# Kernel tuning notes

Measured on AMD Instinct MI355X. Metric: run time of the kernel, lower is better.

The kernel has to match this reference:

```python
import jax, jax.numpy as jnp
import numpy as np

N, T = 128, 20
E_IN, E_EMB, E_RNN = 2, 64, 256
N_IN, N_EMB, N_RNN, N_OUT = 2, 64, 128, 5
ATT = 64

# static edge index sets: diagonal = temporal edges (i,i), off-diagonal = spatial edges (i,j)
_DIAG = np.arange(N) * N + np.arange(N)
_OFFJ = np.array([[j for j in range(N) if j != i] for i in range(N)])  # [N, N-1]
_OFFD = (np.arange(N)[:, None] * N + _OFFJ).reshape(-1)               # [N*(N-1)]
_TEMP = (N - 1) / np.sqrt(ATT)  # attention temperature = num_edges / sqrt(attention_size)


def setup_inputs() -> dict:
    ks = iter(jax.random.split(jax.random.key(0), 40))
    def p(shape, s=0.05):
        return jax.random.normal(next(ks), shape, jnp.float32) * s
    return {
        "nodes": p((T, N, N_IN), 1.0),
        "edges": p((T, N * N, E_IN), 1.0),
        "h_edge0": jnp.zeros((N * N, E_RNN), jnp.float32),
        "c_edge0": jnp.zeros((N * N, E_RNN), jnp.float32),
        "h_node0": jnp.zeros((N, N_RNN), jnp.float32),
        "c_node0": jnp.zeros((N, N_RNN), jnp.float32),
        "t_enc_w": p((E_EMB, E_IN)), "t_enc_b": p((E_EMB,)),
        "t_wih": p((4 * E_RNN, E_EMB)), "t_whh": p((4 * E_RNN, E_RNN)),
        "t_bih": p((4 * E_RNN,)), "t_bhh": p((4 * E_RNN,)),
        "s_enc_w": p((E_EMB, E_IN)), "s_enc_b": p((E_EMB,)),
        "s_wih": p((4 * E_RNN, E_EMB)), "s_whh": p((4 * E_RNN, E_RNN)),
        "s_bih": p((4 * E_RNN,)), "s_bhh": p((4 * E_RNN,)),
        "att_t_w": p((ATT, E_RNN)), "att_t_b": p((ATT,)),
        "att_s_w": p((ATT, E_RNN)), "att_s_b": p((ATT,)),
        "n_enc_w": p((N_EMB, N_IN)), "n_enc_b": p((N_EMB,)),
        "n_attn_w": p((N_EMB, 2 * E_RNN)), "n_attn_b": p((N_EMB,)),
        "n_wih": p((4 * N_RNN, 2 * N_EMB)), "n_whh": p((4 * N_RNN, N_RNN)),
        "n_bih": p((4 * N_RNN,)), "n_bhh": p((4 * N_RNN,)),
        "out_w": p((N_OUT, N_RNN)), "out_b": p((N_OUT,)),
    }


def _lstm(x, h, c, wih, whh, bih, bhh):
    g = x @ wih.T + bih + h @ whh.T + bhh
    i, f, gg, o = jnp.split(g, 4, axis=-1)
    c2 = jax.nn.sigmoid(f) * c + jax.nn.sigmoid(i) * jnp.tanh(gg)
    return jax.nn.sigmoid(o) * jnp.tanh(c2), c2


def reference(nodes, edges, h_edge0, c_edge0, h_node0, c_node0,
              t_enc_w, t_enc_b, t_wih, t_whh, t_bih, t_bhh,
              s_enc_w, s_enc_b, s_wih, s_whh, s_bih, s_bhh,
              att_t_w, att_t_b, att_s_w, att_s_b,
              n_enc_w, n_enc_b, n_attn_w, n_attn_b,
              n_wih, n_whh, n_bih, n_bhh, out_w, out_b):
    def step(carry, xt):
        h_e, c_e, h_n, c_n = carry
        pos_t, edg_t = xt
        # temporal edge RNN on self edges (i,i)
        x_t = jax.nn.relu(edg_t[_DIAG] @ t_enc_w.T + t_enc_b)
        h_t, c_t = _lstm(x_t, h_e[_DIAG], c_e[_DIAG], t_wih, t_whh, t_bih, t_bhh)
        # spatial edge RNN on all pairwise edges (i,j), i != j
        x_s = jax.nn.relu(edg_t[_OFFD] @ s_enc_w.T + s_enc_b)
        h_s, c_s = _lstm(x_s, h_e[_OFFD], c_e[_OFFD], s_wih, s_whh, s_bih, s_bhh)
        h_e = h_e.at[_DIAG].set(h_t).at[_OFFD].set(h_s)
        c_e = c_e.at[_DIAG].set(c_t).at[_OFFD].set(c_s)
        # attention: each node attends over its N-1 spatial edge hidden states
        hs = h_s.reshape(N, N - 1, E_RNN)
        te = h_t @ att_t_w.T + att_t_b                          # [N, ATT]
        se = jnp.einsum('nkd,ad->nka', hs, att_s_w) + att_s_b   # [N, N-1, ATT]
        logits = jnp.einsum('nka,na->nk', se, te) * _TEMP
        w = jax.nn.softmax(logits, axis=-1)
        weighted = jnp.einsum('nk,nkd->nd', w, hs)              # [N, E_RNN]
        # node RNN
        enc = jax.nn.relu(pos_t @ n_enc_w.T + n_enc_b)
        h_edges = jnp.concatenate([h_t, weighted], axis=-1)
        h_emb = jax.nn.relu(h_edges @ n_attn_w.T + n_attn_b)
        h_n, c_n = _lstm(jnp.concatenate([enc, h_emb], axis=-1), h_n, c_n,
                         n_wih, n_whh, n_bih, n_bhh)
        out = h_n @ out_w.T + out_b
        return (h_e, c_e, h_n, c_n), out

    _, outs = jax.lax.scan(step, (h_edge0, c_edge0, h_node0, c_node0), (nodes, edges))
    return outs  # [T, N, 5]
```

## Files before the change

kernel.cpp:

```cpp
#include <hip/hip_runtime.h>
#include <cmath>

#define NN 128
#define TT 20
#define ERNN 256
#define TEMPSC 15.875f

typedef __attribute__((ext_vector_type(8))) short bf16x8;
typedef __attribute__((ext_vector_type(4))) float f32x4;

__device__ __forceinline__ float sigm(float x){ return 1.f/(1.f+__expf(-x)); }
__device__ __forceinline__ float b2f(unsigned short u){ union{unsigned int i; float f;} v; v.i = ((unsigned int)u)<<16; return v.f; }
__device__ __forceinline__ unsigned short f2b(float x){ union{float f; unsigned int u;} v; v.f = x; unsigned int r = v.u + 0x7fffu + ((v.u>>16)&1u); return (unsigned short)(r>>16); }

typedef __attribute__((address_space(3))) unsigned int lds_u32;
typedef __attribute__((address_space(1))) unsigned int glb_u32;
__device__ __forceinline__ void glds16(const void* g, void* l){
    __builtin_amdgcn_global_load_lds((const glb_u32*)g, (lds_u32*)l, 16, 0, 0);
}

__device__ __forceinline__ size_t hoff(int r, int d){
    return ((size_t)((r>>7)*32 + (d>>3))*128 + (r&127))*8 + (d&7);
}

__global__ void k_transpose(const float* __restrict__ s, float* __restrict__ d, int R, int C){
    int i = blockIdx.x*256 + threadIdx.x;
    if (i < R*C){ int r = i / C, c = i - r*C; d[c*R + r] = s[i]; }
}

__global__ void k_bias_sum(const float* __restrict__ a, const float* __restrict__ b,
                           float* __restrict__ o, int n){
    int i = blockIdx.x*256 + threadIdx.x;
    if (i < n) o[i] = a[i] + b[i];
}

__global__ void k_prep_w(const float* __restrict__ wih, const float* __restrict__ whh,
                         unsigned short* __restrict__ wHi){
    int idx = blockIdx.x*256 + threadIdx.x;
    if (idx >= 1024*320) return;
    int c = idx / 320, k = idx - c*320;
    int ch = ((c>>6)<<4) + (c&15), g = (c>>4)&3;
    int r = g*256 + ch;
    float v = (k < 64) ? wih[r*64 + k] : whh[r*256 + (k-64)];
    size_t dst = ((size_t)((c>>7)*40 + (k>>3))*128 + (c&127))*8 + (k&7);
    wHi[dst] = f2b(v);
}

__global__ void k_prep_b(const float* __restrict__ bih, const float* __restrict__ bhh,
                         float* __restrict__ bs){
    int c = blockIdx.x*256 + threadIdx.x;
    if (c < 1024){ int ch = ((c>>6)<<4)+(c&15), g=(c>>4)&3; int r = g*256+ch; bs[c] = bih[r] + bhh[r]; }
}

__global__ void k_prep_xenc(const float* __restrict__ edges,
                            const float* __restrict__ s_enc_w, const float* __restrict__ s_enc_b,
                            const float* __restrict__ t_enc_w, const float* __restrict__ t_enc_b,
                            unsigned short* __restrict__ xe){
    size_t g = (size_t)blockIdx.x*256 + threadIdx.x;
    if (g >= (size_t)TT*16384*8) return;
    int row = (int)(g & 127);
    size_t rest = g >> 7;
    int kc = (int)(rest & 7);
    int tile = (int)((rest >> 3) & 127);
    int t = (int)(rest >> 10);
    int r = tile*128 + row;
    bool sp = (r < 16256);
    int row_ij;
    if (sp) { int i = r/127, jj = r - i*127; row_ij = i*NN + jj + (jj>=i ? 1:0); }
    else    { row_ij = (r - 16256)*(NN+1); }
    const float* w = sp ? s_enc_w : t_enc_w;
    const float* b = sp ? s_enc_b : t_enc_b;
    float e0 = edges[((size_t)t*16384 + row_ij)*2];
    float e1 = edges[((size_t)t*16384 + row_ij)*2 + 1];
    bf16x8 v8;
    #pragma unroll
    for (int q = 0; q < 8; ++q) {
        int m = kc*8 + q;
        v8[q] = (short)f2b(fmaxf(fmaf(w[m*2], e0, fmaf(w[m*2+1], e1, b[m])), 0.f));
    }
    *(bf16x8*)&xe[g*8] = v8;
}

__global__ void k_init_state(const float* __restrict__ h0, const float* __restrict__ c0,
                             unsigned short* __restrict__ hHi, float* __restrict__ c_all){
    int g = blockIdx.x*256 + threadIdx.x;
    if (g >= 16384*32) return;
    int d8 = g & 31, r = g >> 5;
    int row_ij;
    if (r < 16256){ int i = r/127, jj = r - i*127; row_ij = i*NN + jj + (jj>=i ? 1:0); }
    else          { row_ij = (r - 16256)*(NN+1); }
    const float* hs = h0 + (size_t)row_ij*ERNN + d8*8;
    const float* cs = c0 + (size_t)row_ij*ERNN + d8*8;
    bf16x8 hb;
    #pragma unroll
    for (int q = 0; q < 8; ++q) hb[q] = (short)f2b(hs[q]);
    *(bf16x8*)&hHi[hoff(r, d8*8)] = hb;
    float* cd = c_all + (size_t)r*ERNN + d8*8;
    *(float4*)cd       = *(const float4*)cs;
    *(float4*)(cd + 4) = *(const float4*)(cs + 4);
}

__global__ __launch_bounds__(512) void k_fused(
    const unsigned short* __restrict__ xenc_t,
    const unsigned short* __restrict__ h_in, unsigned short* __restrict__ h_out,
    unsigned short* __restrict__ hl_out, float* __restrict__ c_all,
    const unsigned short* __restrict__ s_wHi, const float* __restrict__ s_bs,
    const unsigned short* __restrict__ t_wHi, const float* __restrict__ t_bs,
    int has_node, int n_edge,
    const float* __restrict__ nodes_prev, const unsigned short* __restrict__ hl_prev,
    float* __restrict__ h_nn, float* __restrict__ c_nn, float* __restrict__ out_prev,
    const float* __restrict__ att_t_w, const float* __restrict__ att_t_b,
    const float* __restrict__ att_s_w, const float* __restrict__ att_s_b,
    const float* __restrict__ n_enc_w, const float* __restrict__ n_enc_b,
    const float* __restrict__ n_attn_w, const float* __restrict__ n_attn_b,
    const float* __restrict__ n_wT, const float* __restrict__ n_bsum,
    const float* __restrict__ out_w, const float* __restrict__ out_b)
{
    __shared__ __align__(16) char smem[16384];
    const int bid = blockIdx.x, tid = threadIdx.x;

    if (bid < NN) {
        if (!has_node) return;
        const int i = bid;
        float* sm  = (float*)smem;
        float* ht  = sm;
        float* te  = sm + 256;
        float* u   = sm + 320;
        float* lg  = sm + 576;
        float* cat = sm + 704;
        float* xc  = sm + 1216;
        float* hnl = sm + 1344;
        float* gl  = sm + 1472;
        float* pws = sm + 1984;
        float* msc = sm + 4032;

        if (tid < 256) ht[tid] = b2f(hl_prev[(size_t)(16256 + i)*256 + tid]);
        __syncthreads();
        if (tid < 256) {
            int m = tid >> 2, q = tid & 3;
            float s = 0.f;
            const float* wr = att_t_w + m*ERNN + q*64;
            const float* hh = ht + q*64;
            #pragma unroll 8
            for (int k = 0; k < 64; ++k) s = fmaf(wr[k], hh[k], s);
            s += __shfl_xor(s, 1);
            s += __shfl_xor(s, 2);
            if (q == 0) te[m] = s + att_t_b[m];
        }
        __syncthreads();
        if (tid < 256) {
            float s = 0.f;
            for (int m = 0; m < 64; ++m) s = fmaf(att_s_w[m*ERNN + tid], te[m], s);
            u[tid] = s;
        }
        if (tid == 320) {
            float s = 0.f;
            for (int m = 0; m < 64; ++m) s = fmaf(te[m], att_s_b[m], s);
            msc[2] = s;
        }
        __syncthreads();
        {
            int slot = tid >> 2, q = tid & 3;
            float part = 0.f;
            if (slot < 127) {
                const unsigned short* hs = hl_prev + (size_t)(i*127 + slot)*256 + q*64;
                const float* uu = u + q*64;
                #pragma unroll
                for (int d8 = 0; d8 < 8; ++d8) {
                    bf16x8 v = *(const bf16x8*)(hs + d8*8);
                    #pragma unroll
                    for (int j = 0; j < 8; ++j)
                        part = fmaf(uu[d8*8 + j], b2f((unsigned short)v[j]), part);
                }
            }
            part += __shfl_xor(part, 1);
            part += __shfl_xor(part, 2);
            if (slot < 127 && q == 0) lg[slot] = (part + msc[2]) * TEMPSC;
            if (tid == 511) lg[127] = -1e30f;
        }
        __syncthreads();
        if (tid < 64) {
            float a = fmaxf(lg[tid], lg[tid+64]);
            for (int off = 32; off; off >>= 1) a = fmaxf(a, __shfl_xor(a, off));
            if (tid == 0) msc[0] = a;
        }
        __syncthreads();
        if (tid < 128) lg[tid] = (tid < 127) ? __expf(lg[tid] - msc[0]) : 0.f;
        __syncthreads();
        if (tid < 64) {
            float a = lg[tid] + lg[tid+64];
            for (int off = 32; off; off >>= 1) a += __shfl_xor(a, off);
            if (tid == 0) msc[1] = a;
        }
        __syncthreads();
        {
            int w = tid >> 6, lane = tid & 63;
            float a0 = 0.f, a1 = 0.f, a2 = 0.f, a3 = 0.f;
            #pragma unroll 4
            for (int s = w*16; s < w*16 + 16; ++s) {
                int srow = (s < 127) ? s : 0;
                float wgt = lg[s];
                const unsigned short* hs = hl_prev + (size_t)(i*127 + srow)*256 + lane*4;
                ushort4 v = *(const ushort4*)hs;
                a0 = fmaf(wgt, b2f(v.x), a0);
                a1 = fmaf(wgt, b2f(v.y), a1);
                a2 = fmaf(wgt, b2f(v.z), a2);
                a3 = fmaf(wgt, b2f(v.w), a3);
            }
            pws[w*256 + lane*4+0] = a0; pws[w*256 + lane*4+1] = a1;
            pws[w*256 + lane*4+2] = a2; pws[w*256 + lane*4+3] = a3;
        }
        if (tid >= 256 && tid < 384) hnl[tid-256] = h_nn[i*128 + (tid-256)];
        __syncthreads();
        if (tid < 256) {
            float s = 0.f;
            #pragma unroll
            for (int w = 0; w < 8; ++w) s += pws[w*256 + tid];
            cat[256 + tid] = s / msc[1];
            cat[tid] = ht[tid];
        }
        __syncthreads();
        if (tid < 64) {
            float p0 = nodes_prev[i*2], p1 = nodes_prev[i*2+1];
            xc[tid] = fmaxf(fmaf(n_enc_w[tid*2], p0, fmaf(n_enc_w[tid*2+1], p1, n_enc_b[tid])), 0.f);
        }
        if (tid >= 256) {
            int t2 = tid - 256;
            int m = t2 >> 2, q = t2 & 3;
            float s = 0.f;
            const float* wr = n_attn_w + m*512 + q*128;
            const float* cc = cat + q*128;
            #pragma unroll 8
            for (int d = 0; d < 128; ++d) s = fmaf(wr[d], cc[d], s);
            s += __shfl_xor(s, 1);
            s += __shfl_xor(s, 2);
            if (q == 0) xc[64 + m] = fmaxf(s + n_attn_b[m], 0.f);
        }
        __syncthreads();
        {
            int n = tid;
            float s = n_bsum[n];
            for (int k = 0; k < 128; ++k) s = fmaf(n_wT[k*512 + n], xc[k], s);
            for (int k = 0; k < 128; ++k) s = fmaf(n_wT[(128+k)*512 + n], hnl[k], s);
            gl[n] = s;
        }
        __syncthreads();
        if (tid < 128) {
            float co = c_nn[i*128 + tid];
            float c2 = sigm(gl[128+tid])*co + sigm(gl[tid])*tanhf(gl[256+tid]);
            float h2 = sigm(gl[384+tid])*tanhf(c2);
            c_nn[i*128+tid] = c2;
            h_nn[i*128+tid] = h2;
            hnl[tid] = h2;
        }
        __syncthreads();
        if (tid < 5) {
            float s = out_b[tid];
            const float* wr = out_w + tid*128;
            for (int k = 0; k < 128; ++k) s = fmaf(wr[k], hnl[k], s);
            out_prev[i*5 + tid] = s;
        }
        return;
    }

    if (!n_edge) return;
    unsigned short* Ah = (unsigned short*)smem;
    unsigned short* Bh = (unsigned short*)(smem + 8192);
    const int ebid = bid - NN;
    const int lane = tid & 63, wid = tid >> 6;
    const int wg = (ebid & 7)*128 + (ebid >> 3);
    const int bm = wg >> 3, ntp = wg & 7;
    const bool sp = (bm < 127);
    const int rbase = bm * 128;
    const unsigned short* wHi = sp ? s_wHi : t_wHi;
    const float* bs = sp ? s_bs : t_bs;
    const int wr = wid & 3, wc = wid >> 2;
    const int nt = ntp*2 + wc;

    auto stage = [&](int ks){
        int kc = wid >> 1, half = wid & 1;
        const unsigned short* asrc = (ks < 2)
            ? xenc_t + ((size_t)bm*8  + ks*4     + kc)*1024 + half*512
            : h_in   + ((size_t)bm*32 + (ks-2)*4 + kc)*1024 + half*512;
        glds16(asrc + lane*8, (char*)Ah + wid*1024);
        size_t wb = ((size_t)(ntp*40 + ks*4 + kc)*128 + half*64)*8;
        glds16(wHi + wb + lane*8, (char*)Bh + wid*1024);
    };
    stage(0);

    f32x4 acc[2][4];
    #pragma unroll
    for (int m = 0; m < 2; ++m)
        #pragma unroll
        for (int g = 0; g < 4; ++g)
            acc[m][g] = (f32x4){0.f,0.f,0.f,0.f};

    const int arow = wr*32 + (lane & 15);
    const int bcol = wc*64 + (lane & 15);
    const int kg = lane >> 4;
    for (int ks = 0; ; ++ks) {
        __syncthreads();
        bf16x8 a[2], bb[4];
        #pragma unroll
        for (int m = 0; m < 2; ++m) a[m] = *(const bf16x8*)&Ah[(kg*128 + arow + m*16)*8];
        #pragma unroll
        for (int g = 0; g < 4; ++g) bb[g] = *(const bf16x8*)&Bh[(kg*128 + bcol + g*16)*8];
        #pragma unroll
        for (int m = 0; m < 2; ++m)
            #pragma unroll
            for (int g = 0; g < 4; ++g)
                acc[m][g] = __builtin_amdgcn_mfma_f32_16x16x32_bf16(a[m], bb[g], acc[m][g], 0, 0, 0);
        if (ks == 9) break;
        __syncthreads();
        stage(ks+1);
    }

    const int chl = lane & 15, q4 = (lane >> 4)*4;
    const int ch = nt*16 + chl;
    const int cbase = nt*64 + chl;
    const float b0 = bs[cbase], b1 = bs[cbase+16], b2 = bs[cbase+32], b3 = bs[cbase+48];
    #pragma unroll
    for (int m = 0; m < 2; ++m) {
        #pragma unroll
        for (int rg = 0; rg < 4; ++rg) {
            int lrow = wr*32 + m*16 + q4 + rg;
            int row = rbase + lrow;
            float gi = acc[m][0][rg] + b0;
            float gf = acc[m][1][rg] + b1;
            float gg = acc[m][2][rg] + b2;
            float go = acc[m][3][rg] + b3;
            size_t off = (size_t)row*256 + ch;
            float c_old = c_all[off];
            float c2 = sigm(gf)*c_old + sigm(gi)*tanhf(gg);
            float h2 = sigm(go)*tanhf(c2);
            c_all[off] = c2;
            unsigned short hb = f2b(h2);
            h_out[((size_t)(bm*32 + (ch>>3))*128 + lrow)*8 + (ch&7)] = hb;
            hl_out[off] = hb;
        }
    }
}

extern "C" void kernel_launch(void* const* d_in, const int* in_sizes, int n_in,
                              void* d_out, int out_size, void* d_ws, size_t ws_size,
                              hipStream_t stream)
{
    const float* nodes   = (const float*)d_in[0];
    const float* edges   = (const float*)d_in[1];
    const float* h_e0    = (const float*)d_in[2];
    const float* c_e0    = (const float*)d_in[3];
    const float* h_n0    = (const float*)d_in[4];
    const float* c_n0    = (const float*)d_in[5];
    const float* t_enc_w = (const float*)d_in[6];
    const float* t_enc_b = (const float*)d_in[7];
    const float* t_wih   = (const float*)d_in[8];
    const float* t_whh   = (const float*)d_in[9];
    const float* t_bih   = (const float*)d_in[10];
    const float* t_bhh   = (const float*)d_in[11];
    const float* s_enc_w = (const float*)d_in[12];
    const float* s_enc_b = (const float*)d_in[13];
    const float* s_wih   = (const float*)d_in[14];
    const float* s_whh   = (const float*)d_in[15];
    const float* s_bih   = (const float*)d_in[16];
    const float* s_bhh   = (const float*)d_in[17];
    const float* att_t_w = (const float*)d_in[18];
    const float* att_t_b = (const float*)d_in[19];
    const float* att_s_w = (const float*)d_in[20];
    const float* att_s_b = (const float*)d_in[21];
    const float* n_enc_w = (const float*)d_in[22];
    const float* n_enc_b = (const float*)d_in[23];
    const float* n_attn_w= (const float*)d_in[24];
    const float* n_attn_b= (const float*)d_in[25];
    const float* n_wih   = (const float*)d_in[26];
    const float* n_whh   = (const float*)d_in[27];
    const float* n_bih   = (const float*)d_in[28];
    const float* n_bhh   = (const float*)d_in[29];
    const float* out_w   = (const float*)d_in[30];
    const float* out_b   = (const float*)d_in[31];
    float* out = (float*)d_out;

    char* p = (char*)d_ws;
    float* c_all = (float*)p;            p += (size_t)16384*256*4;
    float* h_nn  = (float*)p;            p += 128*128*4;
    float* c_nn  = (float*)p;            p += 128*128*4;
    float* s_bs  = (float*)p;            p += 1024*4;
    float* t_bs  = (float*)p;            p += 1024*4;
    float* n_wT  = (float*)p;            p += 256*512*4;
    float* n_bs  = (float*)p;            p += 512*4;
    unsigned short* h_a  = (unsigned short*)p;  p += (size_t)16384*256*2;
    unsigned short* h_b  = (unsigned short*)p;  p += (size_t)16384*256*2;
    unsigned short* hl_a = (unsigned short*)p;  p += (size_t)16384*256*2;
    unsigned short* hl_b = (unsigned short*)p;  p += (size_t)16384*256*2;
    unsigned short* xenc = (unsigned short*)p;  p += (size_t)TT*16384*64*2;
    unsigned short* s_wHi = (unsigned short*)p; p += 1024*320*2;
    unsigned short* t_wHi = (unsigned short*)p; p += 1024*320*2;

    hipMemcpyAsync(h_nn, h_n0, 128*128*sizeof(float), hipMemcpyDeviceToDevice, stream);
    hipMemcpyAsync(c_nn, c_n0, 128*128*sizeof(float), hipMemcpyDeviceToDevice, stream);

    k_init_state<<<2048, 256, 0, stream>>>(h_e0, c_e0, h_a, c_all);
    k_prep_w<<<1280, 256, 0, stream>>>(s_wih, s_whh, s_wHi);
    k_prep_w<<<1280, 256, 0, stream>>>(t_wih, t_whh, t_wHi);
    k_prep_b<<<4, 256, 0, stream>>>(s_bih, s_bhh, s_bs);
    k_prep_b<<<4, 256, 0, stream>>>(t_bih, t_bhh, t_bs);
    k_prep_xenc<<<10240, 256, 0, stream>>>(edges, s_enc_w, s_enc_b, t_enc_w, t_enc_b, xenc);
    k_transpose<<<(512*128+255)/256, 256, 0, stream>>>(n_wih, n_wT, 512, 128);
    k_transpose<<<(512*128+255)/256, 256, 0, stream>>>(n_whh, n_wT + 128*512, 512, 128);
    k_bias_sum<<<2, 256, 0, stream>>>(n_bih, n_bhh, n_bs, 512);

    for (int t = 0; t < TT; ++t) {
        const unsigned short* h_in  = (t & 1) ? h_b : h_a;
        unsigned short*       h_out = (t & 1) ? h_a : h_b;
        unsigned short*       hl_out= (t & 1) ? hl_b : hl_a;
        const unsigned short* hl_prev=(t & 1) ? hl_a : hl_b;
        const float* nprev = (t > 0) ? nodes + (size_t)(t-1)*NN*2 : nodes;
        float* oprev = (t > 0) ? out + (size_t)(t-1)*NN*5 : out;
        k_fused<<<NN + 1024, 512, 0, stream>>>(xenc + (size_t)t*16384*64,
            h_in, h_out, hl_out, c_all,
            s_wHi, s_bs, t_wHi, t_bs,
            (t > 0) ? 1 : 0, 1024,
            nprev, hl_prev, h_nn, c_nn, oprev,
            att_t_w, att_t_b, att_s_w, att_s_b, n_enc_w, n_enc_b,
            n_attn_w, n_attn_b, n_wT, n_bs, out_w, out_b);
    }
    k_fused<<<NN, 512, 0, stream>>>(xenc,
        h_a, h_b, hl_a, c_all,
        s_wHi, s_bs, t_wHi, t_bs,
        1, 0,
        nodes + (size_t)19*NN*2, hl_b, h_nn, c_nn, out + (size_t)19*NN*5,
        att_t_w, att_t_b, att_s_w, att_s_b, n_enc_w, n_enc_b,
        n_attn_w, n_attn_b, n_wT, n_bs, out_w, out_b);
}
```

Baseline: 710.9 us.

## Double-buffer edge LSTM GEMM LDS stages and merge weight/bias prep launches

Switches the edge-LSTM MFMA loop from a single LDS buffer to two, prefetching the k-step two ahead with global_load_lds. Explicit vmcnt/lgkmcnt waits and barriers replace the per-step syncthreads pairs. This lets loads overlap the MFMAs. LDS use per block doubles to 32 KB, which may lower occupancy. Separately, the s/t weight and bias prep kernels are merged into single launches to cut launch count.

```diff
diff --git a/kernel.cpp b/kernel.cpp
--- a/kernel.cpp
+++ b/kernel.cpp
@@ -34,10 +34,17 @@
     if (i < n) o[i] = a[i] + b[i];
 }
 
-__global__ void k_prep_w(const float* __restrict__ wih, const float* __restrict__ whh,
-                         unsigned short* __restrict__ wHi){
+__global__ void k_prep_w2(const float* __restrict__ s_wih, const float* __restrict__ s_whh,
+                          unsigned short* __restrict__ s_wHi,
+                          const float* __restrict__ t_wih, const float* __restrict__ t_whh,
+                          unsigned short* __restrict__ t_wHi){
     int idx = blockIdx.x*256 + threadIdx.x;
-    if (idx >= 1024*320) return;
+    if (idx >= 2*1024*320) return;
+    int which = idx >= 1024*320;
+    if (which) idx -= 1024*320;
+    const float* wih = which ? t_wih : s_wih;
+    const float* whh = which ? t_whh : s_whh;
+    unsigned short* wHi = which ? t_wHi : s_wHi;
     int c = idx / 320, k = idx - c*320;
     int ch = ((c>>6)<<4) + (c&15), g = (c>>4)&3;
     int r = g*256 + ch;
@@ -46,10 +53,20 @@
     wHi[dst] = f2b(v);
 }
 
-__global__ void k_prep_b(const float* __restrict__ bih, const float* __restrict__ bhh,
-                         float* __restrict__ bs){
+__global__ void k_prep_b2(const float* __restrict__ s_bih, const float* __restrict__ s_bhh,
+                          float* __restrict__ s_bs,
+                          const float* __restrict__ t_bih, const float* __restrict__ t_bhh,
+                          float* __restrict__ t_bs){
     int c = blockIdx.x*256 + threadIdx.x;
-    if (c < 1024){ int ch = ((c>>6)<<4)+(c&15), g=(c>>4)&3; int r = g*256+ch; bs[c] = bih[r] + bhh[r]; }
+    if (c >= 2048) return;
+    int which = c >= 1024;
+    if (which) c -= 1024;
+    const float* bih = which ? t_bih : s_bih;
+    const float* bhh = which ? t_bhh : s_bhh;
+    float* bs = which ? t_bs : s_bs;
+    int ch = ((c>>6)<<4)+(c&15), g=(c>>4)&3;
+    int r = g*256+ch;
+    bs[c] = bih[r] + bhh[r];
 }
 
 __global__ void k_prep_xenc(const float* __restrict__ edges,
@@ -100,6 +117,30 @@
     *(float4*)(cd + 4) = *(const float4*)(cs + 4);
 }
 
+#define ESTEP(KS, NW) do { \
+    asm volatile("s_waitcnt vmcnt(" #NW ")" ::: "memory"); \
+    __builtin_amdgcn_s_barrier(); \
+    __builtin_amdgcn_sched_barrier(0); \
+    bf16x8 a0 = *(const bf16x8*)&Ah[(KS)&1][(kg*128 + arow)*8]; \
+    bf16x8 a1 = *(const bf16x8*)&Ah[(KS)&1][(kg*128 + arow + 16)*8]; \
+    bf16x8 b0 = *(const bf16x8*)&Bh[(KS)&1][(kg*128 + bcol)*8]; \
+    bf16x8 b1 = *(const bf16x8*)&Bh[(KS)&1][(kg*128 + bcol + 16)*8]; \
+    bf16x8 b2 = *(const bf16x8*)&Bh[(KS)&1][(kg*128 + bcol + 32)*8]; \
+    bf16x8 b3 = *(const bf16x8*)&Bh[(KS)&1][(kg*128 + bcol + 48)*8]; \
+    asm volatile("s_waitcnt lgkmcnt(0)" ::: "memory"); \
+    __builtin_amdgcn_sched_barrier(0); \
+    __builtin_amdgcn_s_barrier(); \
+    if ((KS) + 2 <= 9) stage((KS)+2, (KS)&1); \
+    acc[0][0] = __builtin_amdgcn_mfma_f32_16x16x32_bf16(a0, b0, acc[0][0],0,0,0); \
+    acc[0][1] = __builtin_amdgcn_mfma_f32_16x16x32_bf16(a0, b1, acc[0][1],0,0,0); \
+    acc[0][2] = __builtin_amdgcn_mfma_f32_16x16x32_bf16(a0, b2, acc[0][2],0,0,0); \
+    acc[0][3] = __builtin_amdgcn_mfma_f32_16x16x32_bf16(a0, b3, acc[0][3],0,0,0); \
+    acc[1][0] = __builtin_amdgcn_mfma_f32_16x16x32_bf16(a1, b0, acc[1][0],0,0,0); \
+    acc[1][1] = __builtin_amdgcn_mfma_f32_16x16x32_bf16(a1, b1, acc[1][1],0,0,0); \
+    acc[1][2] = __builtin_amdgcn_mfma_f32_16x16x32_bf16(a1, b2, acc[1][2],0,0,0); \
+    acc[1][3] = __builtin_amdgcn_mfma_f32_16x16x32_bf16(a1, b3, acc[1][3],0,0,0); \
+} while(0)
+
 __global__ __launch_bounds__(512) void k_fused(
     const unsigned short* __restrict__ xenc_t,
     const unsigned short* __restrict__ h_in, unsigned short* __restrict__ h_out,
@@ -116,7 +157,7 @@
     const float* __restrict__ n_wT, const float* __restrict__ n_bsum,
     const float* __restrict__ out_w, const float* __restrict__ out_b)
 {
-    __shared__ __align__(16) char smem[16384];
+    __shared__ __align__(16) char smem[32768];
     const int bid = blockIdx.x, tid = threadIdx.x;
 
     if (bid < NN) {
@@ -264,8 +305,8 @@
     }
 
     if (!n_edge) return;
-    unsigned short* Ah = (unsigned short*)smem;
-    unsigned short* Bh = (unsigned short*)(smem + 8192);
+    unsigned short (*Ah)[4096] = (unsigned short(*)[4096])smem;
+    unsigned short (*Bh)[4096] = (unsigned short(*)[4096])(smem + 16384);
     const int ebid = bid - NN;
     const int lane = tid & 63, wid = tid >> 6;
     const int wg = (ebid & 7)*128 + (ebid >> 3);
@@ -277,16 +318,17 @@
     const int wr = wid & 3, wc = wid >> 2;
     const int nt = ntp*2 + wc;
 
-    auto stage = [&](int ks){
+    auto stage = [&](int ks, int b){
         int kc = wid >> 1, half = wid & 1;
         const unsigned short* asrc = (ks < 2)
             ? xenc_t + ((size_t)bm*8  + ks*4     + kc)*1024 + half*512
             : h_in   + ((size_t)bm*32 + (ks-2)*4 + kc)*1024 + half*512;
-        glds16(asrc + lane*8, (char*)Ah + wid*1024);
+        glds16(asrc + lane*8, (char*)&Ah[b][0] + wid*1024);
         size_t wb = ((size_t)(ntp*40 + ks*4 + kc)*128 + half*64)*8;
-        glds16(wHi + wb + lane*8, (char*)Bh + wid*1024);
+        glds16(wHi + wb + lane*8, (char*)&Bh[b][0] + wid*1024);
     };
-    stage(0);
+    stage(0, 0);
+    stage(1, 1);
 
     f32x4 acc[2][4];
     #pragma unroll
@@ -298,22 +340,17 @@
     const int arow = wr*32 + (lane & 15);
     const int bcol = wc*64 + (lane & 15);
     const int kg = lane >> 4;
-    for (int ks = 0; ; ++ks) {
-        __syncthreads();
-        bf16x8 a[2], bb[4];
-        #pragma unroll
-        for (int m = 0; m < 2; ++m) a[m] = *(const bf16x8*)&Ah[(kg*128 + arow + m*16)*8];
-        #pragma unroll
-        for (int g = 0; g < 4; ++g) bb[g] = *(const bf16x8*)&Bh[(kg*128 + bcol + g*16)*8];
-        #pragma unroll
-        for (int m = 0; m < 2; ++m)
-            #pragma unroll
-            for (int g = 0; g < 4; ++g)
-                acc[m][g] = __builtin_amdgcn_mfma_f32_16x16x32_bf16(a[m], bb[g], acc[m][g], 0, 0, 0);
-        if (ks == 9) break;
-        __syncthreads();
-        stage(ks+1);
-    }
+
+    ESTEP(0, 2);
+    ESTEP(1, 2);
+    ESTEP(2, 2);
+    ESTEP(3, 2);
+    ESTEP(4, 2);
+    ESTEP(5, 2);
+    ESTEP(6, 2);
+    ESTEP(7, 2);
+    ESTEP(8, 2);
+    ESTEP(9, 0);
 
     const int chl = lane & 15, q4 = (lane >> 4)*4;
     const int ch = nt*16 + chl;
@@ -399,10 +436,8 @@
     hipMemcpyAsync(c_nn, c_n0, 128*128*sizeof(float), hipMemcpyDeviceToDevice, stream);
 
     k_init_state<<<2048, 256, 0, stream>>>(h_e0, c_e0, h_a, c_all);
-    k_prep_w<<<1280, 256, 0, stream>>>(s_wih, s_whh, s_wHi);
-    k_prep_w<<<1280, 256, 0, stream>>>(t_wih, t_whh, t_wHi);
-    k_prep_b<<<4, 256, 0, stream>>>(s_bih, s_bhh, s_bs);
-    k_prep_b<<<4, 256, 0, stream>>>(t_bih, t_bhh, t_bs);
+    k_prep_w2<<<2560, 256, 0, stream>>>(s_wih, s_whh, s_wHi, t_wih, t_whh, t_wHi);
+    k_prep_b2<<<8, 256, 0, stream>>>(s_bih, s_bhh, s_bs, t_bih, t_bhh, t_bs);
     k_prep_xenc<<<10240, 256, 0, stream>>>(edges, s_enc_w, s_enc_b, t_enc_w, t_enc_b, xenc);
     k_transpose<<<(512*128+255)/256, 256, 0, stream>>>(n_wih, n_wT, 512, 128);
     k_transpose<<<(512*128+255)/256, 256, 0, stream>>>(n_whh, n_wT + 128*512, 512, 128);
```

After: 640.1 us. -10.0%, faster.
